# Performance work log

Hardware: AMD Instinct MI355X
Metric: run time of the kernel (lower is better)

The kernel has to match this reference:

```python
import jax, jax.numpy as jnp
import numpy as np

N_DELTA, N_THETA, N_GAMMA = 2, 4, 8
N_OSC = N_DELTA + N_THETA + N_GAMMA  # 14
INPUT_DIM = 512
N_CLASSES = 2
COUPLING = 1.5
DT = 0.01
N_STEPS = 100


def _natural_freqs():
    # Natural frequencies (Hz) per EEG band: delta ~2Hz, theta ~6Hz, gamma ~40Hz
    return jnp.concatenate([
        jnp.full((N_DELTA,), 2.0, dtype=jnp.float32),
        jnp.full((N_THETA,), 6.0, dtype=jnp.float32),
        jnp.full((N_GAMMA,), 40.0, dtype=jnp.float32),
    ])


def setup_inputs() -> dict:
    key = jax.random.key(0)
    k_x, k_win, k_wc = jax.random.split(key, 3)
    x = jax.random.normal(k_x, (4096, 64, INPUT_DIM), dtype=jnp.float32)
    W_in = jax.random.normal(k_win, (INPUT_DIM, N_OSC), dtype=jnp.float32) / np.sqrt(INPUT_DIM)
    b_in = jnp.zeros((N_OSC,), dtype=jnp.float32)
    omega = _natural_freqs()
    Wc = jax.random.normal(k_wc, (N_OSC, N_CLASSES), dtype=jnp.float32) / np.sqrt(N_OSC)
    bc = jnp.zeros((N_CLASSES,), dtype=jnp.float32)
    return {"x": x, "W_in": W_in, "b_in": b_in, "omega": omega, "Wc": Wc, "bc": bc}


def reference(x, W_in, b_in, omega, Wc, bc):
    # Mean-pool over the object/token dimension: [B,S,D] -> [B,D]
    if x.ndim == 3:
        x = x.mean(axis=1)
    # Project input features to initial oscillator phases: [B,14]
    theta0 = x @ W_in + b_in
    two_pi = jnp.float32(2.0 * np.pi)
    k_over_n = jnp.float32(COUPLING / N_OSC)
    dt = jnp.float32(DT)

    def step(theta, _):
        s = jnp.sin(theta)
        c = jnp.cos(theta)
        # mean-field Kuramoto coupling: sum_j sin(th_j - th_i) = S*cos(th_i) - C*sin(th_i)
        S = s.sum(axis=-1, keepdims=True)
        C = c.sum(axis=-1, keepdims=True)
        dtheta = two_pi * omega + k_over_n * (S * c - C * s)
        return theta + dt * dtheta, None

    theta, _ = jax.lax.scan(step, theta0, None, length=N_STEPS)
    h = jnp.cos(theta)  # oscillator readout: [B,14]
    logits = h @ Wc + bc
    return jax.nn.log_softmax(logits, axis=-1)
```

## Files before the change

kernel.cpp:

```cpp
#include <hip/hip_runtime.h>
#include <math.h>

#define SEQ   64
#define DIM   512
#define NOSC  14
#define NSTEP 100
#define RPB   4

typedef float f4 __attribute__((ext_vector_type(4)));

__device__ __forceinline__ float dpp_sum4(float v) {
    v += __int_as_float(__builtin_amdgcn_update_dpp(0, __float_as_int(v), 0xB1,  0xF, 0xF, true));
    v += __int_as_float(__builtin_amdgcn_update_dpp(0, __float_as_int(v), 0x4E,  0xF, 0xF, true));
    return v;
}
__device__ __forceinline__ float dpp_sum16(float v) {
    v += __int_as_float(__builtin_amdgcn_update_dpp(0, __float_as_int(v), 0xB1,  0xF, 0xF, true));
    v += __int_as_float(__builtin_amdgcn_update_dpp(0, __float_as_int(v), 0x4E,  0xF, 0xF, true));
    v += __int_as_float(__builtin_amdgcn_update_dpp(0, __float_as_int(v), 0x141, 0xF, 0xF, true));
    v += __int_as_float(__builtin_amdgcn_update_dpp(0, __float_as_int(v), 0x140, 0xF, 0xF, true));
    return v;
}

__device__ __forceinline__ void fast_sincos(float theta, float* s, float* c) {
    const float inv2pi = 0.15915494309189535f;
    float r = theta * inv2pi;
    r = r - floorf(r);
    *s = __builtin_amdgcn_sinf(r);
    *c = __builtin_amdgcn_cosf(r);
}

__global__ __launch_bounds__(256, 4)
void fused_kernel(const float* __restrict__ x,
                  const float* __restrict__ W_in,
                  const float* __restrict__ b_in,
                  const float* __restrict__ omega,
                  const float* __restrict__ Wc,
                  const float* __restrict__ bc,
                  float* __restrict__ out, int B)
{
    const int t    = threadIdx.x;
    const int wv   = t >> 6;
    const int ln   = t & 63;
    const int row0 = blockIdx.x * RPB;

    __shared__ f4    mvbuf[2][2][DIM / 4];
    __shared__ float th0[RPB][16];
    __shared__ int   flags[RPB];

    if (t < RPB) flags[t] = 0;
    __syncthreads();

    if (wv < 2) {
        const int o = ln >> 2;
        const int q = ln & 3;
        for (int rr = 0; rr < RPB / 2; ++rr) {
            const int r   = wv + 2 * rr;
            const int row = row0 + r;
            if (row >= B) break;

            const f4* xv = reinterpret_cast<const f4*>(x + (size_t)row * (SEQ * DIM));
            f4 a0 = (f4)(0.0f), a1 = (f4)(0.0f);
#pragma unroll 8
            for (int s = 0; s < SEQ; ++s) {
                a0 += __builtin_nontemporal_load(&xv[s * (DIM / 4) + ln]);
                a1 += __builtin_nontemporal_load(&xv[s * (DIM / 4) + 64 + ln]);
            }
            f4* mw = mvbuf[wv][rr & 1];
            mw[ln]      = a0 * (1.0f / SEQ);
            mw[ln + 64] = a1 * (1.0f / SEQ);
            asm volatile("s_waitcnt lgkmcnt(0)" ::: "memory");

            const float* m = reinterpret_cast<const float*>(mw);
            float p = 0.f;
            if (o < NOSC) {
#pragma unroll 16
                for (int i = 0; i < 128; ++i) {
                    const int d = q * 128 + i;
                    p += m[d] * W_in[d * NOSC + o];
                }
            }
            p = dpp_sum4(p);
            if (q == 0) th0[r][o] = (o < NOSC) ? (p + b_in[o]) : 0.f;
            if (ln == 0)
                __hip_atomic_store(&flags[r], 1, __ATOMIC_RELEASE, __HIP_MEMORY_SCOPE_WORKGROUP);
        }
    } else if (wv == 3) {
        const int grp = ln >> 4;
        const int o   = ln & 15;
        const int row = row0 + grp;
        if (row < B) {
            while (__hip_atomic_load(&flags[grp], __ATOMIC_ACQUIRE, __HIP_MEMORY_SCOPE_WORKGROUP) == 0)
                __builtin_amdgcn_s_sleep(4);

            const bool  act  = (o < NOSC);
            const float mask = act ? 1.0f : 0.0f;
            const int   oc   = act ? o : (NOSC - 1);

            float theta = th0[grp][o];
            const float drift = 6.283185307179586f * omega[oc];
            const float kn = 1.5f / (float)NOSC;
            const float dt = 0.01f;

            for (int it = 0; it < NSTEP; ++it) {
                float s_, c_;
                fast_sincos(theta, &s_, &c_);
                s_ *= mask; c_ *= mask;
                const float S = dpp_sum16(s_);
                const float C = dpp_sum16(c_);
                theta += dt * (drift + kn * (S * c_ - C * s_));
            }

            float hs, hc;
            fast_sincos(theta, &hs, &hc);
            const float h = hc * mask;
            float z0 = dpp_sum16(h * Wc[oc * 2 + 0]);
            float z1 = dpp_sum16(h * Wc[oc * 2 + 1]);
            if (o == 0) {
                z0 += bc[0]; z1 += bc[1];
                const float mx  = fmaxf(z0, z1);
                const float lse = mx + logf(expf(z0 - mx) + expf(z1 - mx));
                out[(size_t)row * 2 + 0] = z0 - lse;
                out[(size_t)row * 2 + 1] = z1 - lse;
            }
        }
    }
}

extern "C" void kernel_launch(void* const* d_in, const int* in_sizes, int n_in,
                              void* d_out, int out_size, void* d_ws, size_t ws_size,
                              hipStream_t stream)
{
    const float* x     = (const float*)d_in[0];
    const float* W_in  = (const float*)d_in[1];
    const float* b_in  = (const float*)d_in[2];
    const float* omega = (const float*)d_in[3];
    const float* Wc    = (const float*)d_in[4];
    const float* bc    = (const float*)d_in[5];
    float* out = (float*)d_out;

    const int B = in_sizes[0] / (SEQ * DIM);

    const int grid = (B + RPB - 1) / RPB;
    fused_kernel<<<grid, 256, 0, stream>>>(x, W_in, b_in, omega, Wc, bc, out, B);
}
```

Measured before the change: 99.69 us.

## Give each wave its own row end-to-end, dropping producer/consumer flag handoff

Each of the four waves in a block now streams one full row of x, does the projection, and runs the Kuramoto integration itself. This replaces the old scheme, where two waves loaded two rows each and a third wave spun on shared-memory flags to integrate all four rows. The aim is to use all four waves for the bandwidth-bound load and to remove the serialization and sleep-polling between producer and consumer. The W_in dot-product index is rotated per quarter to spread LDS bank access, and the output is written as a single float2. The cost is that every wave now runs the serial 100-step oscillator loop redundantly across its 64 lanes, where 16 lanes would do.

```diff
diff --git a/kernel.cpp b/kernel.cpp
--- a/kernel.cpp
+++ b/kernel.cpp
@@ -39,91 +39,76 @@
                   const float* __restrict__ bc,
                   float* __restrict__ out, int B)
 {
-    const int t    = threadIdx.x;
-    const int wv   = t >> 6;
-    const int ln   = t & 63;
-    const int row0 = blockIdx.x * RPB;
+    const int t   = threadIdx.x;
+    const int wv  = t >> 6;
+    const int ln  = t & 63;
+    const int row = blockIdx.x * RPB + wv;
 
-    __shared__ f4    mvbuf[2][2][DIM / 4];
+    __shared__ f4    mv[RPB][DIM / 4];
     __shared__ float th0[RPB][16];
-    __shared__ int   flags[RPB];
 
-    if (t < RPB) flags[t] = 0;
-    __syncthreads();
+    if (row >= B) return;
 
-    if (wv < 2) {
+    const f4* xv = reinterpret_cast<const f4*>(x + (size_t)row * (SEQ * DIM));
+    f4 a0 = (f4)(0.0f), a1 = (f4)(0.0f);
+#pragma unroll 8
+    for (int s = 0; s < SEQ; ++s) {
+        a0 += __builtin_nontemporal_load(&xv[s * (DIM / 4) + ln]);
+        a1 += __builtin_nontemporal_load(&xv[s * (DIM / 4) + 64 + ln]);
+    }
+    f4* mw = mv[wv];
+    mw[ln]      = a0 * (1.0f / SEQ);
+    mw[ln + 64] = a1 * (1.0f / SEQ);
+    asm volatile("s_waitcnt lgkmcnt(0)" ::: "memory");
+
+    {
+        const float* m = reinterpret_cast<const float*>(mw);
         const int o = ln >> 2;
         const int q = ln & 3;
-        for (int rr = 0; rr < RPB / 2; ++rr) {
-            const int r   = wv + 2 * rr;
-            const int row = row0 + r;
-            if (row >= B) break;
-
-            const f4* xv = reinterpret_cast<const f4*>(x + (size_t)row * (SEQ * DIM));
-            f4 a0 = (f4)(0.0f), a1 = (f4)(0.0f);
-#pragma unroll 8
-            for (int s = 0; s < SEQ; ++s) {
-                a0 += __builtin_nontemporal_load(&xv[s * (DIM / 4) + ln]);
-                a1 += __builtin_nontemporal_load(&xv[s * (DIM / 4) + 64 + ln]);
-            }
-            f4* mw = mvbuf[wv][rr & 1];
-            mw[ln]      = a0 * (1.0f / SEQ);
-            mw[ln + 64] = a1 * (1.0f / SEQ);
-            asm volatile("s_waitcnt lgkmcnt(0)" ::: "memory");
-
-            const float* m = reinterpret_cast<const float*>(mw);
-            float p = 0.f;
-            if (o < NOSC) {
+        float p = 0.f;
+        if (o < NOSC) {
 #pragma unroll 16
-                for (int i = 0; i < 128; ++i) {
-                    const int d = q * 128 + i;
-                    p += m[d] * W_in[d * NOSC + o];
-                }
-            }
-            p = dpp_sum4(p);
-            if (q == 0) th0[r][o] = (o < NOSC) ? (p + b_in[o]) : 0.f;
-            if (ln == 0)
-                __hip_atomic_store(&flags[r], 1, __ATOMIC_RELEASE, __HIP_MEMORY_SCOPE_WORKGROUP);
-        }
-    } else if (wv == 3) {
-        const int grp = ln >> 4;
-        const int o   = ln & 15;
-        const int row = row0 + grp;
-        if (row < B) {
-            while (__hip_atomic_load(&flags[grp], __ATOMIC_ACQUIRE, __HIP_MEMORY_SCOPE_WORKGROUP) == 0)
-                __builtin_amdgcn_s_sleep(4);
-
-            const bool  act  = (o < NOSC);
-            const float mask = act ? 1.0f : 0.0f;
-            const int   oc   = act ? o : (NOSC - 1);
-
-            float theta = th0[grp][o];
-            const float drift = 6.283185307179586f * omega[oc];
-            const float kn = 1.5f / (float)NOSC;
-            const float dt = 0.01f;
-
-            for (int it = 0; it < NSTEP; ++it) {
-                float s_, c_;
-                fast_sincos(theta, &s_, &c_);
-                s_ *= mask; c_ *= mask;
-                const float S = dpp_sum16(s_);
-                const float C = dpp_sum16(c_);
-                theta += dt * (drift + kn * (S * c_ - C * s_));
-            }
-
-            float hs, hc;
-            fast_sincos(theta, &hs, &hc);
-            const float h = hc * mask;
-            float z0 = dpp_sum16(h * Wc[oc * 2 + 0]);
-            float z1 = dpp_sum16(h * Wc[oc * 2 + 1]);
-            if (o == 0) {
-                z0 += bc[0]; z1 += bc[1];
-                const float mx  = fmaxf(z0, z1);
-                const float lse = mx + logf(expf(z0 - mx) + expf(z1 - mx));
-                out[(size_t)row * 2 + 0] = z0 - lse;
-                out[(size_t)row * 2 + 1] = z1 - lse;
+            for (int i = 0; i < 128; ++i) {
+                const int d = q * 128 + ((i + 8 * q) & 127);
+                p += m[d] * W_in[d * NOSC + o];
             }
         }
+        p = dpp_sum4(p);
+        if (q == 0) th0[wv][o] = (o < NOSC) ? (p + b_in[o]) : 0.f;
+    }
+    asm volatile("s_waitcnt lgkmcnt(0)" ::: "memory");
+
+    const int  o    = ln & 15;
+    const bool act  = (o < NOSC);
+    const float mask = act ? 1.0f : 0.0f;
+    const int   oc   = act ? o : (NOSC - 1);
+
+    float theta = th0[wv][o];
+    const float drift = 6.283185307179586f * omega[oc];
+    const float kn = 1.5f / (float)NOSC;
+    const float dt = 0.01f;
+
+    for (int it = 0; it < NSTEP; ++it) {
+        float s_, c_;
+        fast_sincos(theta, &s_, &c_);
+        s_ *= mask; c_ *= mask;
+        const float S = dpp_sum16(s_);
+        const float C = dpp_sum16(c_);
+        theta += dt * (drift + kn * (S * c_ - C * s_));
+    }
+
+    float hs, hc;
+    fast_sincos(theta, &hs, &hc);
+    const float h = hc * mask;
+    float z0 = dpp_sum16(h * Wc[oc * 2 + 0]);
+    float z1 = dpp_sum16(h * Wc[oc * 2 + 1]);
+
+    if (ln == 0) {
+        z0 += bc[0]; z1 += bc[1];
+        const float mx  = fmaxf(z0, z1);
+        const float lse = mx + logf(expf(z0 - mx) + expf(z1 - mx));
+        float2 r = make_float2(z0 - lse, z1 - lse);
+        *reinterpret_cast<float2*>(&out[(size_t)row * 2]) = r;
     }
 }
 
```

New measurement: 100.5 us. Within noise of the previous version (+0.8%).
